# Kernel optimization log

Measured on AMD Instinct MI355X. Metric: run time of the kernel, lower is better.

The kernel has to match this reference:

```python
import jax, jax.numpy as jnp
import numpy as np

LODS = [16, 32, 64, 128, 256]
SCENE_SCALE = 4.0
DESC = 4
N = 2_000_000
# 8 corner offsets of a voxel, bit-decoded: (x, y, z) in {0,1}^3
_CORNERS = jnp.asarray([[(i >> 2) & 1, (i >> 1) & 1, i & 1] for i in range(8)], dtype=jnp.int32)  # (8,3)


def setup_inputs() -> dict:
    key = jax.random.key(0)
    ks = jax.random.split(key, 2 + len(LODS))
    inp = {
        "pts": jax.random.normal(ks[0], (N, 3), dtype=jnp.float32),
        "d": jax.random.normal(ks[1], (N, 3), dtype=jnp.float32),
    }
    # codebook init mirrors torch: zeros + 0.01 * randn, shape (LOD^3, desc)
    for i, res in enumerate(LODS):
        inp[f"codebook_{i}"] = jax.random.normal(ks[2 + i], (res ** 3, DESC), dtype=jnp.float32) * 0.01
    return inp


def _trilerp(res, codebook, pts01):
    """NGLOD-style dense-grid trilinear interpolation.
    pts01: (N,3) in [0,1]; codebook: (res^3, DESC). Returns (N, DESC)."""
    pos = pts01 * (res - 1)                                   # (N,3) in [0, res-1]
    c0 = jnp.clip(jnp.floor(pos).astype(jnp.int32), 0, res - 2)
    frac = pos - c0.astype(pos.dtype)                         # (N,3) in [0,1]
    idx = c0[:, None, :] + _CORNERS[None, :, :]               # (N,8,3)
    flat = (idx[..., 0] * res + idx[..., 1]) * res + idx[..., 2]  # (N,8) row-major x*res^2+y*res+z
    # trilinear weights: prod over axes of (frac if corner bit set else 1-frac)
    w = jnp.prod(jnp.where(_CORNERS[None] == 1, frac[:, None, :], 1.0 - frac[:, None, :]), axis=-1)  # (N,8)
    return jnp.einsum('nkd,nk->nd', codebook[flat], w)        # gather + weighted sum


def reference(pts, d, codebook_0, codebook_1, codebook_2, codebook_3, codebook_4):
    cbs = (codebook_0, codebook_1, codebook_2, codebook_3, codebook_4)
    p = pts / SCENE_SCALE
    mask = jnp.all(jnp.abs(p) < 0.5, axis=-1)                 # inside unit cube
    p01 = jnp.clip(p + 0.5, 0.0, 1.0)                         # clamp keeps OOB points index-safe; masked out below
    feats = _trilerp(LODS[0], cbs[0], p01)
    for res, cb in zip(LODS[1:], cbs[1:]):
        feats = feats + _trilerp(res, cb, p01)                # sum features across LODs
    color = jnp.where(mask[:, None], feats[:, 0:3], 0.0)      # masked scatter into zero buffer
    log_sigma = jnp.where(mask, feats[:, 3], -100000.0)       # exp(-1e5) underflows to 0, as in torch
    return color, jnp.exp(log_sigma)[:, None]
```

## Files before the change

### kernel.cpp

```cpp
#include <hip/hip_runtime.h>
#include <math.h>

static constexpr float kSceneScale = 4.0f;
static constexpr int   kG     = 16;
static constexpr int   kNBins = kG * kG * kG + 1;
static constexpr int   kNB    = 256;
static constexpr int   kDirectThresh = 48;
static constexpr int   kS4 = 17;

__device__ __forceinline__ void fma4(float4& acc, float w, const float4& c) {
    acc.x = fmaf(w, c.x, acc.x);
    acc.y = fmaf(w, c.y, acc.y);
    acc.z = fmaf(w, c.z, acc.z);
    acc.w = fmaf(w, c.w, acc.w);
}

__device__ __forceinline__ unsigned bf16r(float f) {
    unsigned u = __float_as_uint(f);
    return (u + 0x7FFFu + ((u >> 16) & 1u)) >> 16;
}
__device__ __forceinline__ unsigned pk2(float lo, float hi) {
    return bf16r(lo) | (bf16r(hi) << 16);
}
__device__ __forceinline__ float4 bfdec(uint2 w) {
    float4 r;
    r.x = __uint_as_float(w.x << 16);
    r.y = __uint_as_float(w.x & 0xFFFF0000u);
    r.z = __uint_as_float(w.y << 16);
    r.w = __uint_as_float(w.y & 0xFFFF0000u);
    return r;
}

template <int RES>
__device__ __forceinline__ void trilerp_acc(const float4* __restrict__ cb,
                                            float x, float y, float z,
                                            float4& acc) {
    const float s = (float)(RES - 1);
    float fx = x * s, fy = y * s, fz = z * s;
    int x0 = min((int)fx, RES - 2);
    int y0 = min((int)fy, RES - 2);
    int z0 = min((int)fz, RES - 2);
    float tx = fx - (float)x0;
    float ty = fy - (float)y0;
    float tz = fz - (float)z0;
    int base = (x0 * RES + y0) * RES + z0;
    float4 c000 = cb[base];
    float4 c001 = cb[base + 1];
    float4 c010 = cb[base + RES];
    float4 c011 = cb[base + RES + 1];
    float4 c100 = cb[base + RES * RES];
    float4 c101 = cb[base + RES * RES + 1];
    float4 c110 = cb[base + RES * RES + RES];
    float4 c111 = cb[base + RES * RES + RES + 1];
    float wx0 = 1.0f - tx, wx1 = tx;
    float wy0 = 1.0f - ty, wy1 = ty;
    float wz0 = 1.0f - tz, wz1 = tz;
    fma4(acc, wx0 * wy0 * wz0, c000);
    fma4(acc, wx0 * wy0 * wz1, c001);
    fma4(acc, wx0 * wy1 * wz0, c010);
    fma4(acc, wx0 * wy1 * wz1, c011);
    fma4(acc, wx1 * wy0 * wz0, c100);
    fma4(acc, wx1 * wy0 * wz1, c101);
    fma4(acc, wx1 * wy1 * wz0, c110);
    fma4(acc, wx1 * wy1 * wz1, c111);
}

__device__ __forceinline__ void load_p01(const float* __restrict__ pts, int i,
                                         float& x, float& y, float& z, bool& inside) {
    float px = pts[3 * i + 0] * (1.0f / kSceneScale);
    float py = pts[3 * i + 1] * (1.0f / kSceneScale);
    float pz = pts[3 * i + 2] * (1.0f / kSceneScale);
    inside = (fabsf(px) < 0.5f) && (fabsf(py) < 0.5f) && (fabsf(pz) < 0.5f);
    x = fminf(fmaxf(px + 0.5f, 0.0f), 1.0f);
    y = fminf(fmaxf(py + 0.5f, 0.0f), 1.0f);
    z = fminf(fmaxf(pz + 0.5f, 0.0f), 1.0f);
}

__device__ __forceinline__ unsigned point_key(const float* __restrict__ pts, int i) {
    float x, y, z; bool inside;
    load_p01(pts, i, x, y, z, inside);
    if (!inside) return (unsigned)(kNBins - 1);
    int x0 = min((int)(x * 255.0f), 254) >> 4;
    int y0 = min((int)(y * 255.0f), 254) >> 4;
    int z0 = min((int)(z * 255.0f), 254) >> 4;
    return (unsigned)((x0 * kG + y0) * kG + z0);
}

__global__ __launch_bounds__(256) void keys_hist_kernel(
        const float* __restrict__ pts, unsigned* __restrict__ keys,
        unsigned* __restrict__ blockHist, int n, int chunk) {
    __shared__ unsigned hist[kNBins];
    int tid = threadIdx.x;
    for (int j = tid; j < kNBins; j += 256) hist[j] = 0;
    __syncthreads();
    int beg = blockIdx.x * chunk;
    int end = min(n, beg + chunk);
    for (int i = beg + tid; i < end; i += 256) {
        unsigned key = point_key(pts, i);
        keys[i] = key;
        atomicAdd(&hist[key], 1u);
    }
    __syncthreads();
    for (int j = tid; j < kNBins; j += 256) blockHist[(size_t)j * kNB + blockIdx.x] = hist[j];
}

__global__ __launch_bounds__(256) void scan_chunks_kernel(
        unsigned* __restrict__ data, unsigned* __restrict__ partials, int total) {
    __shared__ unsigned sums[256];
    int tid = threadIdx.x;
    int base = blockIdx.x * 1024 + tid * 4;
    uint4 v = make_uint4(0u, 0u, 0u, 0u);
    if (base + 3 < total) {
        v = *(const uint4*)(data + base);
    } else {
        unsigned* p = (unsigned*)&v;
        for (int k = 0; k < 4; ++k) if (base + k < total) p[k] = data[base + k];
    }
    unsigned s1 = v.x + v.y, s2 = s1 + v.z, s3 = s2 + v.w;
    sums[tid] = s3;
    __syncthreads();
    for (int off = 1; off < 256; off <<= 1) {
        unsigned t = (tid >= off) ? sums[tid - off] : 0u;
        __syncthreads();
        sums[tid] += t;
        __syncthreads();
    }
    unsigned excl = sums[tid] - s3;
    uint4 o;
    o.x = excl; o.y = excl + v.x; o.z = excl + s1; o.w = excl + s2;
    if (base + 3 < total) {
        *(uint4*)(data + base) = o;
    } else {
        unsigned* p = (unsigned*)&o;
        for (int k = 0; k < 4; ++k) if (base + k < total) data[base + k] = p[k];
    }
    if (tid == 255) partials[blockIdx.x] = sums[255];
}

__global__ __launch_bounds__(256) void scan_partials_kernel(unsigned* __restrict__ partials, int m) {
    __shared__ unsigned buf[256];
    __shared__ unsigned carry_s;
    int tid = threadIdx.x;
    if (tid == 0) carry_s = 0u;
    __syncthreads();
    for (int base = 0; base < m; base += 256) {
        unsigned v = (base + tid < m) ? partials[base + tid] : 0u;
        buf[tid] = v;
        __syncthreads();
        for (int off = 1; off < 256; off <<= 1) {
            unsigned t = (tid >= off) ? buf[tid - off] : 0u;
            __syncthreads();
            buf[tid] += t;
            __syncthreads();
        }
        unsigned incl = buf[tid];
        unsigned c = carry_s;
        if (base + tid < m) partials[base + tid] = c + incl - v;
        __syncthreads();
        if (tid == 255) carry_s = c + incl;
        __syncthreads();
    }
}

__global__ __launch_bounds__(256) void scan_add_kernel(
        unsigned* __restrict__ data, const unsigned* __restrict__ partials, int total) {
    int tid = threadIdx.x;
    int base = blockIdx.x * 1024 + tid * 4;
    unsigned p = partials[blockIdx.x];
    if (base + 3 < total) {
        uint4 v = *(const uint4*)(data + base);
        v.x += p; v.y += p; v.z += p; v.w += p;
        *(uint4*)(data + base) = v;
    } else {
        for (int k = 0; k < 4; ++k) if (base + k < total) data[base + k] += p;
    }
}

__global__ __launch_bounds__(256) void scatter_kernel(
        const float* __restrict__ pts,
        const unsigned* __restrict__ keys, const unsigned* __restrict__ blockHist,
        float4* __restrict__ spts, float* __restrict__ out, int n, int chunk) {
    __shared__ unsigned offs[kNBins];
    int tid = threadIdx.x;
    for (int j = tid; j < kNBins; j += 256) offs[j] = blockHist[(size_t)j * kNB + blockIdx.x];
    __syncthreads();
    int beg = blockIdx.x * chunk;
    int end = min(n, beg + chunk);
    for (int i = beg + tid; i < end; i += 256) {
        unsigned k = keys[i];
        float x, y, z; bool inside;
        load_p01(pts, i, x, y, z, inside);
        unsigned pos = atomicAdd(&offs[k], 1u);
        if (inside) {
            spts[pos] = make_float4(x, y, z, __uint_as_float((unsigned)i));
        } else {
            out[3 * i + 0] = 0.0f;
            out[3 * i + 1] = 0.0f;
            out[3 * i + 2] = 0.0f;
            out[(size_t)3 * n + i] = 0.0f;
        }
    }
}

__global__ __launch_bounds__(512, 8) void compute_tiled_kernel(
        const float4* __restrict__ spts,
        const unsigned* __restrict__ blockHist,
        const float4* __restrict__ cb0,
        const float4* __restrict__ cb1,
        const float4* __restrict__ cb2,
        const float4* __restrict__ cb3,
        const float4* __restrict__ cb4,
        float* __restrict__ out,
        int n) {
    int bin = blockIdx.x;
    unsigned start = blockHist[(size_t)bin * kNB];
    unsigned end   = blockHist[(size_t)(bin + 1) * kNB];
    if (start >= end) return;

    int tid = threadIdx.x;

    if ((int)(end - start) < kDirectThresh) {
        for (unsigned t = start + tid; t < end; t += 512) {
            float4 s = spts[t];
            int i = (int)__float_as_uint(s.w);
            float4 acc = make_float4(0.0f, 0.0f, 0.0f, 0.0f);
            trilerp_acc<16>(cb0, s.x, s.y, s.z, acc);
            trilerp_acc<32>(cb1, s.x, s.y, s.z, acc);
            trilerp_acc<64>(cb2, s.x, s.y, s.z, acc);
            trilerp_acc<128>(cb3, s.x, s.y, s.z, acc);
            trilerp_acc<256>(cb4, s.x, s.y, s.z, acc);
            out[3 * i + 0] = acc.x;
            out[3 * i + 1] = acc.y;
            out[3 * i + 2] = acc.z;
            out[(size_t)3 * n + i] = expf(acc.w);
        }
        return;
    }

    __shared__ uint2 s4[kS4 * kS4 * kS4];

    int bx = bin >> 8, by = (bin >> 4) & 15, bz = bin & 15;
    int ox = bx << 4, oy = by << 4, oz = bz << 4;

    for (int c = tid; c < kS4 * kS4 * kS4; c += 512) {
        int cz = c % kS4;
        int cy = (c / kS4) % kS4;
        int cx = c / (kS4 * kS4);
        int gx = min(ox + cx, 255);
        int gy = min(oy + cy, 255);
        int gz = min(oz + cz, 255);
        float4 v = cb4[((size_t)gx * 256 + gy) * 256 + gz];
        s4[c] = make_uint2(pk2(v.x, v.y), pk2(v.z, v.w));
    }
    __syncthreads();

    for (unsigned t = start + tid; t < end; t += 512) {
        float4 s = spts[t];
        int i = (int)__float_as_uint(s.w);
        float4 acc = make_float4(0.0f, 0.0f, 0.0f, 0.0f);
        trilerp_acc<16>(cb0, s.x, s.y, s.z, acc);
        trilerp_acc<32>(cb1, s.x, s.y, s.z, acc);
        trilerp_acc<64>(cb2, s.x, s.y, s.z, acc);
        trilerp_acc<128>(cb3, s.x, s.y, s.z, acc);

        {
            float fx = s.x * 255.0f, fy = s.y * 255.0f, fz = s.z * 255.0f;
            int x0 = min((int)fx, 254);
            int y0 = min((int)fy, 254);
            int z0 = min((int)fz, 254);
            float tx = fx - (float)x0;
            float ty = fy - (float)y0;
            float tz = fz - (float)z0;
            int base = ((x0 - ox) * kS4 + (y0 - oy)) * kS4 + (z0 - oz);
            uint2 w000 = s4[base];
            uint2 w001 = s4[base + 1];
            uint2 w010 = s4[base + kS4];
            uint2 w011 = s4[base + kS4 + 1];
            uint2 w100 = s4[base + kS4 * kS4];
            uint2 w101 = s4[base + kS4 * kS4 + 1];
            uint2 w110 = s4[base + kS4 * kS4 + kS4];
            uint2 w111 = s4[base + kS4 * kS4 + kS4 + 1];
            float wx0 = 1.0f - tx, wx1 = tx;
            float wy0 = 1.0f - ty, wy1 = ty;
            float wz0 = 1.0f - tz, wz1 = tz;
            fma4(acc, wx0 * wy0 * wz0, bfdec(w000));
            fma4(acc, wx0 * wy0 * wz1, bfdec(w001));
            fma4(acc, wx0 * wy1 * wz0, bfdec(w010));
            fma4(acc, wx0 * wy1 * wz1, bfdec(w011));
            fma4(acc, wx1 * wy0 * wz0, bfdec(w100));
            fma4(acc, wx1 * wy0 * wz1, bfdec(w101));
            fma4(acc, wx1 * wy1 * wz0, bfdec(w110));
            fma4(acc, wx1 * wy1 * wz1, bfdec(w111));
        }

        out[3 * i + 0] = acc.x;
        out[3 * i + 1] = acc.y;
        out[3 * i + 2] = acc.z;
        out[(size_t)3 * n + i] = expf(acc.w);
    }
}

__global__ __launch_bounds__(256) void direct_kernel(
        const float* __restrict__ pts,
        const float4* __restrict__ cb0,
        const float4* __restrict__ cb1,
        const float4* __restrict__ cb2,
        const float4* __restrict__ cb3,
        const float4* __restrict__ cb4,
        float* __restrict__ out,
        int n) {
    int i = blockIdx.x * blockDim.x + threadIdx.x;
    if (i >= n) return;
    float x, y, z; bool inside;
    load_p01(pts, i, x, y, z, inside);
    float c0 = 0.0f, c1 = 0.0f, c2 = 0.0f, sg = 0.0f;
    if (inside) {
        float4 acc = make_float4(0.0f, 0.0f, 0.0f, 0.0f);
        trilerp_acc<16>(cb0, x, y, z, acc);
        trilerp_acc<32>(cb1, x, y, z, acc);
        trilerp_acc<64>(cb2, x, y, z, acc);
        trilerp_acc<128>(cb3, x, y, z, acc);
        trilerp_acc<256>(cb4, x, y, z, acc);
        c0 = acc.x; c1 = acc.y; c2 = acc.z; sg = expf(acc.w);
    }
    out[3 * i + 0] = c0;
    out[3 * i + 1] = c1;
    out[3 * i + 2] = c2;
    out[(size_t)3 * n + i] = sg;
}

extern "C" void kernel_launch(void* const* d_in, const int* in_sizes, int n_in,
                              void* d_out, int out_size, void* d_ws, size_t ws_size,
                              hipStream_t stream) {
    const float* pts = (const float*)d_in[0];
    const float4* cb0 = (const float4*)d_in[2];
    const float4* cb1 = (const float4*)d_in[3];
    const float4* cb2 = (const float4*)d_in[4];
    const float4* cb3 = (const float4*)d_in[5];
    const float4* cb4 = (const float4*)d_in[6];
    float* out = (float*)d_out;

    int n = in_sizes[0] / 3;

    const int histTotal = kNBins * kNB;
    const int nChunks   = (histTotal + 1023) / 1024;

    size_t off_keys = 0;
    size_t off_spts = (off_keys + (size_t)n * 4 + 15) & ~(size_t)15;
    size_t off_hist = off_spts + (size_t)n * 16;
    size_t off_part = off_hist + (size_t)histTotal * 4;
    size_t need     = off_part + (size_t)nChunks * 4;

    dim3 block(256);
    int nwg = (n + 255) / 256;

    if (ws_size < need) {
        direct_kernel<<<dim3(nwg), block, 0, stream>>>(pts, cb0, cb1, cb2, cb3, cb4, out, n);
        return;
    }

    unsigned* keys      = (unsigned*)((char*)d_ws + off_keys);
    float4*   spts      = (float4*)((char*)d_ws + off_spts);
    unsigned* blockHist = (unsigned*)((char*)d_ws + off_hist);
    unsigned* partials  = (unsigned*)((char*)d_ws + off_part);

    int chunk = (n + kNB - 1) / kNB;

    keys_hist_kernel<<<dim3(kNB), block, 0, stream>>>(pts, keys, blockHist, n, chunk);
    scan_chunks_kernel<<<dim3(nChunks), block, 0, stream>>>(blockHist, partials, histTotal);
    scan_partials_kernel<<<dim3(1), block, 0, stream>>>(partials, nChunks);
    scan_add_kernel<<<dim3(nChunks), block, 0, stream>>>(blockHist, partials, histTotal);
    scatter_kernel<<<dim3(kNB), block, 0, stream>>>(pts, keys, blockHist, spts, out, n, chunk);
    compute_tiled_kernel<<<dim3(kG * kG * kG), dim3(512), 0, stream>>>(
        spts, blockHist, cb0, cb1, cb2, cb3, cb4, out, n);
}
```

Baseline: 317.8 us.

## Split dense bins into fixed-size work items for load-balanced tiled compute

Adds a single-block kernel that turns each non-empty spatial bin into chunks of up to 512 points and writes a compact work-item list. The tiled compute kernel then launches one block per work item instead of one per bin, so heavily populated central bins no longer serialize on a single block. The cost is that each chunk reloads the 17^3 LOD-4 shared tile, and there is an extra launch plus a serial single-block builder.

Measured after the change: 303.7 us. 4.4% less time.

```diff
diff --git a/kernel.cpp b/kernel.cpp
--- a/kernel.cpp
+++ b/kernel.cpp
@@ -6,7 +6,8 @@
 static constexpr int   kNBins = kG * kG * kG + 1;
 static constexpr int   kNB    = 256;
 static constexpr int   kDirectThresh = 48;
-static constexpr int   kS4 = 17;
+static constexpr int   kS4    = 17;
+static constexpr int   kChunk = 512;
 
 __device__ __forceinline__ void fma4(float4& acc, float w, const float4& c) {
     acc.x = fmaf(w, c.x, acc.x);
@@ -202,9 +203,31 @@
     }
 }
 
+__global__ __launch_bounds__(512) void build_work_kernel(
+        const unsigned* __restrict__ blockHist,
+        uint2* __restrict__ items, unsigned* __restrict__ numItems) {
+    __shared__ unsigned counter;
+    if (threadIdx.x == 0) counter = 0u;
+    __syncthreads();
+    for (int bin = threadIdx.x; bin < kG * kG * kG; bin += 512) {
+        unsigned s = blockHist[(size_t)bin * kNB];
+        unsigned e = blockHist[(size_t)(bin + 1) * kNB];
+        unsigned cnt = e - s;
+        if (cnt == 0u) continue;
+        unsigned k = (cnt + kChunk - 1) / kChunk;
+        unsigned base = atomicAdd(&counter, k);
+        for (unsigned j = 0; j < k; ++j)
+            items[base + j] = make_uint2((unsigned)bin, s + j * kChunk);
+    }
+    __syncthreads();
+    if (threadIdx.x == 0) numItems[0] = counter;
+}
+
 __global__ __launch_bounds__(512, 8) void compute_tiled_kernel(
         const float4* __restrict__ spts,
         const unsigned* __restrict__ blockHist,
+        const uint2* __restrict__ items,
+        const unsigned* __restrict__ numItems,
         const float4* __restrict__ cb0,
         const float4* __restrict__ cb1,
         const float4* __restrict__ cb2,
@@ -212,10 +235,12 @@
         const float4* __restrict__ cb4,
         float* __restrict__ out,
         int n) {
-    int bin = blockIdx.x;
-    unsigned start = blockHist[(size_t)bin * kNB];
-    unsigned end   = blockHist[(size_t)(bin + 1) * kNB];
-    if (start >= end) return;
+    if (blockIdx.x >= numItems[0]) return;
+    uint2 it = items[blockIdx.x];
+    int bin = (int)it.x;
+    unsigned start = it.y;
+    unsigned binEnd = blockHist[(size_t)(bin + 1) * kNB];
+    unsigned end = min(binEnd, start + (unsigned)kChunk);
 
     int tid = threadIdx.x;
 
@@ -254,7 +279,8 @@
     }
     __syncthreads();
 
-    for (unsigned t = start + tid; t < end; t += 512) {
+    unsigned t = start + tid;
+    if (t < end) {
         float4 s = spts[t];
         int i = (int)__float_as_uint(s.w);
         float4 acc = make_float4(0.0f, 0.0f, 0.0f, 0.0f);
@@ -344,12 +370,15 @@
 
     const int histTotal = kNBins * kNB;
     const int nChunks   = (histTotal + 1023) / 1024;
-
-    size_t off_keys = 0;
-    size_t off_spts = (off_keys + (size_t)n * 4 + 15) & ~(size_t)15;
-    size_t off_hist = off_spts + (size_t)n * 16;
-    size_t off_part = off_hist + (size_t)histTotal * 4;
-    size_t need     = off_part + (size_t)nChunks * 4;
+    const int maxItems  = kG * kG * kG + (n + kChunk - 1) / kChunk;
+
+    size_t off_keys  = 0;
+    size_t off_spts  = (off_keys + (size_t)n * 4 + 15) & ~(size_t)15;
+    size_t off_hist  = off_spts + (size_t)n * 16;
+    size_t off_part  = off_hist + (size_t)histTotal * 4;
+    size_t off_items = (off_part + (size_t)nChunks * 4 + 7) & ~(size_t)7;
+    size_t off_nitem = off_items + (size_t)maxItems * 8;
+    size_t need      = off_nitem + 4;
 
     dim3 block(256);
     int nwg = (n + 255) / 256;
@@ -363,6 +392,8 @@
     float4*   spts      = (float4*)((char*)d_ws + off_spts);
     unsigned* blockHist = (unsigned*)((char*)d_ws + off_hist);
     unsigned* partials  = (unsigned*)((char*)d_ws + off_part);
+    uint2*    items     = (uint2*)((char*)d_ws + off_items);
+    unsigned* numItems  = (unsigned*)((char*)d_ws + off_nitem);
 
     int chunk = (n + kNB - 1) / kNB;
 
@@ -371,6 +402,7 @@
     scan_partials_kernel<<<dim3(1), block, 0, stream>>>(partials, nChunks);
     scan_add_kernel<<<dim3(nChunks), block, 0, stream>>>(blockHist, partials, histTotal);
     scatter_kernel<<<dim3(kNB), block, 0, stream>>>(pts, keys, blockHist, spts, out, n, chunk);
-    compute_tiled_kernel<<<dim3(kG * kG * kG), dim3(512), 0, stream>>>(
-        spts, blockHist, cb0, cb1, cb2, cb3, cb4, out, n);
-}
+    build_work_kernel<<<dim3(1), dim3(512), 0, stream>>>(blockHist, items, numItems);
+    compute_tiled_kernel<<<dim3(maxItems), dim3(512), 0, stream>>>(
+        spts, blockHist, items, numItems, cb0, cb1, cb2, cb3, cb4, out, n);
+}
```
